# Kernel optimization log

Hardware: AMD Instinct MI355X
Metric: run time of the kernel (lower is better)

The kernel has to match this reference:

```python
import jax, jax.numpy as jnp
import numpy as np

B, C, H, W = 64, 256, 14, 14
K = 9
HID = 256   # EdgeAgg hidden_channels = in_channels
OUT = 512   # out_channels = 2*in_channels (required by final reshape)


def _knn(q, kset, k):
    # ViG dense_knn_matrix: squared-distance knn, top-k of -dist (self-loop may be included)
    qs = jnp.sum(q * q, -1)
    ks = jnp.sum(kset * kset, -1)
    dist = qs[:, :, None] - 2.0 * jnp.einsum('bnc,bmc->bnm', q, kset) + ks[:, None, :]
    _, idx = jax.lax.top_k(-dist, k)   # (B,N,k) neighbor indices into kset
    return idx


def _edgeconv_add(feat, nbr, validf, w, b):
    # PyG EdgeConv(nn=Linear, aggr='add') with per-node valid-edge mask:
    #   out[i] = sum_{j in valid nbrs(i)} cat(x_i, x_j - x_i) @ w + b
    # nn is linear, so aggregate neighbor diffs BEFORE the matmul (same math, less traffic).
    Cf = feat.shape[-1]
    wa, wb = w[:Cf], w[Cf:]
    deg = jnp.sum(validf, -1, keepdims=True)                   # (B,N,1)
    xj = feat[jnp.arange(feat.shape[0])[:, None, None], nbr]   # (B,N,k,C) gather
    sum_xj = jnp.einsum('bnkc,bnk->bnc', xj, validf)
    return deg * (feat @ wa + b) + (sum_xj - deg * feat) @ wb


def _forward(x, fc1_w, fc1_b, fc2_w, fc2_b, fce_w, fce_b, inout_w, inout_b,
             attn_w, attn_b, upd_w, upd_b, kp_w, kp_b, enc_w, enc_b,
             mu_w, mu_b, dec_w, dec_b, T):
    k = dec_w.shape[-1]
    b_, c_, h_, w_ = x.shape
    n = h_ * w_
    xs = x.reshape(b_, c_, n)                       # (B,C,N)
    x_sp = jnp.transpose(xs, (0, 2, 1))             # (B,N,C) true spatial node feats for knn
    x_sp_d = jax.lax.stop_gradient(x_sp)            # original detaches before knn
    x_nbr = _knn(x_sp_d, x_sp_d, k)
    # temporal roll across the T frames of each clip
    y_sp = jnp.roll(x_sp.reshape(b_ // T, T, n, c_), -1, axis=1).reshape(b_, n, c_)
    y_nbr = _knn(x_sp_d, jax.lax.stop_gradient(y_sp), k)
    # faithful to original: x.view(B*N, C) reinterprets the contiguous (B,C,N) buffer
    x_feat = xs.reshape(b_, n, c_)
    y_feat = jnp.transpose(y_sp, (0, 2, 1)).reshape(b_, n, c_)
    # VAE-like K predictor (deterministic z = mu); argmax -> per-node degree in [0,k)
    hk = x_feat.reshape(b_ * n, c_) @ kp_w + kp_b
    hk = jax.nn.relu(hk @ enc_w + enc_b)
    mu = hk @ mu_w + mu_b
    logits = mu @ dec_w + dec_b                     # (B*N, k)
    k_int = jnp.argmax(logits, axis=1)
    # generate_mask: keep the first k_int[i] of node i's k edges
    validf = (jnp.arange(k)[None, :] < k_int[:, None]).astype(x.dtype).reshape(b_, n, k)

    def edge_agg(feat, nbr):
        h1 = jax.nn.relu(_edgeconv_add(feat, nbr, validf, fc1_w, fc1_b))
        h2 = _edgeconv_add(h1, nbr, validf, fc2_w, fc2_b)
        return (h2 @ fce_w + fce_b).reshape(b_ * n, -1)

    x_agg = edge_agg(x_feat, x_nbr)
    y_agg = edge_agg(y_feat, y_nbr)
    scores = (jnp.concatenate([x_agg, y_agg], -1) @ attn_w + attn_b)[:, 0]
    wgt = jax.nn.softmax(scores, axis=0)[:, None]   # softmax over ALL B*N nodes (as in source)
    fused = wgt * x_agg + (1.0 - wgt) * y_agg
    xin = x_feat.reshape(b_ * n, c_) @ inout_w + inout_b
    upd = jax.nn.relu(jnp.concatenate([xin, fused], -1) @ upd_w + upd_b)   # (B*N, 2C)
    return jnp.transpose(upd.reshape(b_, n, 2 * c_), (0, 2, 1)).reshape(b_, 2 * c_, h_, w_)


def setup_inputs():
    key = jax.random.key(0)
    ks = iter(jax.random.split(key, 32))

    def lin(i, o):
        return jax.random.normal(next(ks), (i, o), jnp.float32) / np.sqrt(i)

    def bias(o):
        return jax.random.normal(next(ks), (o,), jnp.float32) * 0.01

    return {
        'x': jax.random.normal(next(ks), (B, C, H, W), jnp.float32),
        'fc1_w': lin(2 * C, HID), 'fc1_b': bias(HID),
        'fc2_w': lin(2 * HID, HID), 'fc2_b': bias(HID),
        'fce_w': lin(HID, OUT), 'fce_b': bias(OUT),
        'inout_w': lin(C, OUT), 'inout_b': bias(OUT),
        'attn_w': lin(2 * OUT, 1), 'attn_b': bias(1),
        'upd_w': lin(2 * OUT, OUT), 'upd_b': bias(OUT),
        'kp_w': lin(C, 500), 'kp_b': bias(500),
        'enc_w': lin(500, 64), 'enc_b': bias(64),
        'mu_w': lin(64, 32), 'mu_b': bias(32),
        'dec_w': lin(32, K), 'dec_b': bias(K),
        'T': 16,
    }


def reference(x, fc1_w, fc1_b, fc2_w, fc2_b, fce_w, fce_b, inout_w, inout_b,
              attn_w, attn_b, upd_w, upd_b, kp_w, kp_b, enc_w, enc_b,
              mu_w, mu_b, dec_w, dec_b, T):
    return _forward(x, fc1_w, fc1_b, fc2_w, fc2_b, fce_w, fce_b, inout_w, inout_b,
                    attn_w, attn_b, upd_w, upd_b, kp_w, kp_b, enc_w, enc_b,
                    mu_w, mu_b, dec_w, dec_b, T)
```

## Files before the change

### kernel.cpp

```cpp
#include <hip/hip_runtime.h>
#include <cstddef>
#include <cstdint>

constexpr int BATCH = 64;
constexpr int CH    = 256;
constexpr int NPT   = 196;
constexpr int ROWS  = BATCH * NPT;
constexpr int BSTRIDE = CH * NPT;
constexpr int KNB   = 8;

typedef __bf16 bf16x8 __attribute__((ext_vector_type(8)));
typedef __bf16 bf16x4 __attribute__((ext_vector_type(4)));
typedef _Float16 f16x8 __attribute__((ext_vector_type(8)));
typedef float  f32x4  __attribute__((ext_vector_type(4)));

__device__ __forceinline__ int src_batch(int b) {
    return (b & ~15) | ((b + 1) & 15);
}

__device__ __forceinline__ void gload_lds16(const void* g, void* l) {
    __builtin_amdgcn_global_load_lds(
        (const __attribute__((address_space(1))) void*)g,
        (__attribute__((address_space(3))) void*)l, 16, 0, 0);
}

__global__ __launch_bounds__(256) void qs_kernel(const float* __restrict__ x,
                                                 float* __restrict__ qs) {
    int b = blockIdx.x;
    int m = threadIdx.x;
    if (m >= NPT) return;
    const float* xb = x + (size_t)b * BSTRIDE;
    float acc = 0.f;
    for (int c = 0; c < CH; ++c) {
        float v = xb[c * NPT + m];
        acc = fmaf(v, v, acc);
    }
    qs[b * NPT + m] = acc;
}

__global__ __launch_bounds__(256) void trans_split(const float* __restrict__ x,
        _Float16* __restrict__ XH, _Float16* __restrict__ XL,
        __bf16* __restrict__ XB) {
    __shared__ float tile[64][65];
    int b = blockIdx.z;
    int m0 = blockIdx.x * 64, c0 = blockIdx.y * 64;
    int t = threadIdx.x;
    const float* xb = x + (size_t)b * BSTRIDE;
    #pragma unroll
    for (int s = 0; s < 16; ++s) {
        int idx = s * 256 + t;
        int cc = idx >> 6, mm = idx & 63;
        int m = m0 + mm;
        float v = (m < NPT) ? xb[(size_t)(c0 + cc) * NPT + m] : 0.f;
        tile[cc][mm] = v;
        if (m < NPT)
            XB[(size_t)b * BSTRIDE + (size_t)(c0 + cc) * NPT + m] = (__bf16)v;
    }
    __syncthreads();
    #pragma unroll
    for (int s = 0; s < 16; ++s) {
        int idx = s * 256 + t;
        int mm = idx >> 6, cc = idx & 63;
        float v = tile[cc][mm];
        _Float16 h = (_Float16)v;
        size_t off = ((size_t)b * 256 + (m0 + mm)) * 256 + c0 + cc;
        XH[off] = h;
        XL[off] = (_Float16)(v - (float)h);
    }
}

__global__ __launch_bounds__(256) void gram_mfma(const _Float16* __restrict__ XH,
        const _Float16* __restrict__ XL, float* __restrict__ D) {
    __shared__ __attribute__((aligned(16))) _Float16 Ah[128 * 64];
    __shared__ __attribute__((aligned(16))) _Float16 Al[128 * 64];
    __shared__ __attribute__((aligned(16))) _Float16 Bh[128 * 64];
    __shared__ __attribute__((aligned(16))) _Float16 Bl[128 * 64];
    int job = blockIdx.z;
    int qb = (job < 64) ? job : job - 64;
    int kb = (job < 64) ? qb : src_batch(qb);
    int t = threadIdx.x, w = t >> 6, l = t & 63;
    int r0 = blockIdx.y * 128, c0 = blockIdx.x * 128;
    int lr = l & 15, lg = l >> 4;
    int wr = (w >> 1) * 64, wc = (w & 1) * 64;
    const _Float16* qh = XH + (size_t)qb * 65536;
    const _Float16* ql = XL + (size_t)qb * 65536;
    const _Float16* kh = XH + (size_t)kb * 65536;
    const _Float16* kl = XL + (size_t)kb * 65536;
    f32x4 acc[4][4] = {};
    for (int k0 = 0; k0 < 256; k0 += 64) {
        #pragma unroll
        for (int i = 0; i < 4; ++i) {
            int row = (w * 4 + i) * 8 + (l >> 3);
            int c8 = l & 7;
            size_t goA = (size_t)(r0 + row) * 256 + k0 + c8 * 8;
            size_t goB = (size_t)(c0 + row) * 256 + k0 + c8 * 8;
            gload_lds16(qh + goA, Ah + (w * 4 + i) * 512);
            gload_lds16(ql + goA, Al + (w * 4 + i) * 512);
            gload_lds16(kh + goB, Bh + (w * 4 + i) * 512);
            gload_lds16(kl + goB, Bl + (w * 4 + i) * 512);
        }
        asm volatile("s_waitcnt vmcnt(0)" ::: "memory");
        __syncthreads();
        #pragma unroll
        for (int ks = 0; ks < 2; ++ks) {
            f16x8 ah[4], al[4], bh[4], bl[4];
            #pragma unroll
            for (int mi = 0; mi < 4; ++mi) {
                ah[mi] = *(const f16x8*)(Ah + (wr + mi * 16 + lr) * 64 + ks * 32 + lg * 8);
                al[mi] = *(const f16x8*)(Al + (wr + mi * 16 + lr) * 64 + ks * 32 + lg * 8);
            }
            #pragma unroll
            for (int ni = 0; ni < 4; ++ni) {
                bh[ni] = *(const f16x8*)(Bh + (wc + ni * 16 + lr) * 64 + ks * 32 + lg * 8);
                bl[ni] = *(const f16x8*)(Bl + (wc + ni * 16 + lr) * 64 + ks * 32 + lg * 8);
            }
            #pragma unroll
            for (int mi = 0; mi < 4; ++mi)
                #pragma unroll
                for (int ni = 0; ni < 4; ++ni) {
                    acc[mi][ni] = __builtin_amdgcn_mfma_f32_16x16x32_f16(
                        ah[mi], bh[ni], acc[mi][ni], 0, 0, 0);
                    acc[mi][ni] = __builtin_amdgcn_mfma_f32_16x16x32_f16(
                        ah[mi], bl[ni], acc[mi][ni], 0, 0, 0);
                    acc[mi][ni] = __builtin_amdgcn_mfma_f32_16x16x32_f16(
                        al[mi], bh[ni], acc[mi][ni], 0, 0, 0);
                }
        }
        __syncthreads();
    }
    #pragma unroll
    for (int mi = 0; mi < 4; ++mi) {
        #pragma unroll
        for (int r = 0; r < 4; ++r) {
            int gi = r0 + wr + mi * 16 + lg * 4 + r;
            if (gi >= NPT) continue;
            #pragma unroll
            for (int ni = 0; ni < 4; ++ni) {
                int gj = c0 + wc + ni * 16 + lr;
                if (gj < NPT)
                    D[(size_t)job * (NPT * NPT) + (size_t)gi * NPT + gj] =
                        acc[mi][ni][r];
            }
        }
    }
}

__global__ __launch_bounds__(256) void topk_kernel(const float* __restrict__ D,
                                                   const float* __restrict__ qs,
                                                   int* __restrict__ nbr) {
    int wid = threadIdx.x >> 6;
    int lane = threadIdx.x & 63;
    int rowid = blockIdx.x * 4 + wid;
    int job = rowid / NPT;
    int i = rowid - job * NPT;
    int qb = (job < 64) ? job : job - 64;
    int kb = (job < 64) ? qb : src_batch(qb);
    const float* drow = D + (size_t)job * (NPT * NPT) + (size_t)i * NPT;
    float qsi = qs[qb * NPT + i];
    const float* ksr = qs + kb * NPT;
    float dist[4];
    #pragma unroll
    for (int s = 0; s < 4; ++s) {
        int m = lane + 64 * s;
        dist[s] = (m < NPT) ? (qsi - 2.f * drow[m] + ksr[m])
                            : __uint_as_float(0x7f800000u);
    }
    for (int it = 0; it < KNB; ++it) {
        unsigned long long best = ~0ull;
        #pragma unroll
        for (int s = 0; s < 4; ++s) {
            unsigned u = __float_as_uint(dist[s]);
            u = (u & 0x80000000u) ? ~u : (u | 0x80000000u);
            unsigned long long key = ((unsigned long long)u << 32) |
                                     (unsigned)(lane + 64 * s);
            if (key < best) best = key;
        }
        #pragma unroll
        for (int off = 32; off; off >>= 1) {
            unsigned long long o = __shfl_xor(best, off, 64);
            if (o < best) best = o;
        }
        int widx = (int)(best & 0xffffffffu);
        if (lane == (widx & 63)) dist[widx >> 6] = __uint_as_float(0x7f800000u);
        if (lane == 0) nbr[(size_t)rowid * KNB + it] = widx;
    }
}

__global__ __launch_bounds__(256) void compose_all(const float* __restrict__ kp_w,
        const float* __restrict__ kp_b, const float* __restrict__ enc_w,
        const float* __restrict__ enc_b, const float* __restrict__ mu_w,
        const float* __restrict__ mu_b, const float* __restrict__ dec_w,
        const float* __restrict__ dec_b, const float* __restrict__ inout_w,
        const float* __restrict__ inout_b, const float* __restrict__ upd_w,
        const float* __restrict__ upd_b,
        float* __restrict__ KW1, float* __restrict__ kb1,
        float* __restrict__ KW2, float* __restrict__ kb2,
        __bf16* __restrict__ updC, float* __restrict__ bcomp) {
    int bid = blockIdx.x;
    if (bid < 64) {
        int i = bid * 4 + (threadIdx.x >> 6);
        int j = threadIdx.x & 63;
        double acc = 0.0;
        for (int k = 0; k < 500; ++k)
            acc += (double)kp_w[(size_t)i * 500 + k] * (double)enc_w[(size_t)k * 64 + j];
        KW1[i * 64 + j] = (float)acc;
    } else if (bid == 64) {
        int j = threadIdx.x;
        if (j < 64) {
            double acc = (double)enc_b[j];
            for (int k = 0; k < 500; ++k)
                acc += (double)kp_b[k] * (double)enc_w[(size_t)k * 64 + j];
            kb1[j] = (float)acc;
        }
    } else if (bid < 68) {
        int t = (bid - 65) * 256 + threadIdx.x;
        if (t < 576) {
            int i = t / 9, j = t - (t / 9) * 9;
            double acc = 0.0;
            for (int k = 0; k < 32; ++k)
                acc += (double)mu_w[(size_t)i * 32 + k] * (double)dec_w[(size_t)k * 9 + j];
            KW2[t] = (float)acc;
        } else if (t < 585) {
            int j = t - 576;
            double acc = (double)dec_b[j];
            for (int k = 0; k < 32; ++k)
                acc += (double)mu_b[k] * (double)dec_w[(size_t)k * 9 + j];
            kb2[j] = (float)acc;
        }
    } else if (bid < 580) {
        int e = (bid - 68) * 256 + threadIdx.x;
        int k = e >> 9, n = e & 511;
        double acc = 0.0;
        for (int j = 0; j < 512; ++j)
            acc += (double)inout_w[(size_t)k * 512 + j] * (double)upd_w[(size_t)j * 512 + n];
        updC[(size_t)n * 768 + k] = (__bf16)(float)acc;
    } else {
        int n = (bid - 580) * 256 + threadIdx.x;
        double acc = (double)upd_b[n];
        for (int j = 0; j < 512; ++j)
            acc += (double)inout_b[j] * (double)upd_w[(size_t)j * 512 + n];
        bcomp[n] = (float)acc;
    }
}

__global__ __launch_bounds__(256) void kint2_kernel(const float* __restrict__ x,
    const float* __restrict__ W1, const float* __restrict__ b1,
    const float* __restrict__ W2, const float* __restrict__ b2,
    int* __restrict__ kint, float* __restrict__ degf) {
    __shared__ __attribute__((aligned(16))) float xr[16][256];
    __shared__ float ebuf[16][64];
    __shared__ float lg[16][9];
    int t = threadIdx.x;
    int r0 = blockIdx.x * 16;
    const float4* xg = (const float4*)(x + (size_t)r0 * 256);
    float4* xs = (float4*)&xr[0][0];
    #pragma unroll
    for (int s = 0; s < 4; ++s) xs[s * 256 + t] = xg[s * 256 + t];
    __syncthreads();
    int w = t >> 6, l = t & 63;
    {
        float bb = b1[l];
        float a0 = bb, a1 = bb, a2 = bb, a3 = bb;
        const float* x0 = xr[w * 4 + 0];
        const float* x1 = xr[w * 4 + 1];
        const float* x2 = xr[w * 4 + 2];
        const float* x3 = xr[w * 4 + 3];
        for (int c = 0; c < 256; ++c) {
            float wv = W1[c * 64 + l];
            a0 = fmaf(x0[c], wv, a0);
            a1 = fmaf(x1[c], wv, a1);
            a2 = fmaf(x2[c], wv, a2);
            a3 = fmaf(x3[c], wv, a3);
        }
        ebuf[w * 4 + 0][l] = fmaxf(a0, 0.f);
        ebuf[w * 4 + 1][l] = fmaxf(a1, 0.f);
        ebuf[w * 4 + 2][l] = fmaxf(a2, 0.f);
        ebuf[w * 4 + 3][l] = fmaxf(a3, 0.f);
    }
    __syncthreads();
    int rr = t >> 4, cc = t & 15;
    if (cc < 9) {
        float acc = b2[cc];
        for (int j = 0; j < 64; ++j)
            acc = fmaf(ebuf[rr][j], W2[j * 9 + cc], acc);
        lg[rr][cc] = acc;
    }
    __syncthreads();
    if (cc == 0) {
        float best = lg[rr][0];
        int bi = 0;
        #pragma unroll
        for (int j = 1; j < 9; ++j)
            if (lg[rr][j] > best) { best = lg[rr][j]; bi = j; }
        kint[r0 + rr] = bi;
        degf[r0 + rr] = (float)bi;
    }
}

template<int STAGE, int RELU>
__global__ __launch_bounds__(256) void combine_kernel(const __bf16* __restrict__ P,
        const int* __restrict__ nbr, const int* __restrict__ kint_,
        const float* __restrict__ degf, const float* __restrict__ bias,
        __bf16* __restrict__ H) {
    int g = threadIdx.x >> 6, lane = threadIdx.x & 63;
    int r = blockIdx.x * 4 + g;
    int branch = (r >= ROWS);
    int rr = r - branch * ROWS;
    int b = rr / NPT, i = rr - b * NPT;
    size_t srow, mbase;
    if constexpr (STAGE == 1) {
        int fb = branch ? src_batch(b) : b;
        srow = (size_t)fb * NPT + i;
        mbase = (size_t)fb * NPT;
    } else {
        srow = (size_t)r;
        mbase = (size_t)branch * ROWS + (size_t)b * NPT;
    }
    const int* nb = nbr + (size_t)branch * ((size_t)ROWS * KNB) + (size_t)rr * KNB;
    bf16x4 sv = *(const bf16x4*)(P + srow * 512 + lane * 4);
    float4 bv = *(const float4*)(bias + lane * 4);
    float s0 = 0.f, s1 = 0.f, s2 = 0.f, s3 = 0.f;
    int kk = kint_[rr];
    for (int tt = 0; tt < kk; ++tt) {
        int m = nb[tt];
        bf16x4 v = *(const bf16x4*)(P + (mbase + m) * 512 + 256 + lane * 4);
        s0 += (float)v[0]; s1 += (float)v[1]; s2 += (float)v[2]; s3 += (float)v[3];
    }
    float dg = degf[rr];
    float o0 = fmaf(dg, (float)sv[0] + bv.x, s0);
    float o1 = fmaf(dg, (float)sv[1] + bv.y, s1);
    float o2 = fmaf(dg, (float)sv[2] + bv.z, s2);
    float o3 = fmaf(dg, (float)sv[3] + bv.w, s3);
    if constexpr (RELU) {
        o0 = fmaxf(o0, 0.f); o1 = fmaxf(o1, 0.f);
        o2 = fmaxf(o2, 0.f); o3 = fmaxf(o3, 0.f);
    }
    bf16x4 ov;
    ov[0] = (__bf16)o0; ov[1] = (__bf16)o1; ov[2] = (__bf16)o2; ov[3] = (__bf16)o3;
    *(bf16x4*)(H + (size_t)r * 256 + lane * 4) = ov;
}

template<int FLAGS, int CONCAT>
__global__ __launch_bounds__(256) void mfma_gemm(
    const __bf16* __restrict__ A0, const __bf16* __restrict__ A1,
    const __bf16* __restrict__ WT, const float* __restrict__ bias,
    float* __restrict__ Cf, __bf16* __restrict__ Cb, int K, int N,
    const float* __restrict__ aw, float* __restrict__ scp,
    const float* __restrict__ wgt) {
    constexpr int SMEMB = (FLAGS & 8) ? (128 * 129 * 4) : (2 * 128 * 64 * 2);
    __shared__ __attribute__((aligned(16))) char smem[SMEMB];
    __bf16* As = (__bf16*)smem;
    __bf16* Bs = As + 128 * 64;
    int t = threadIdx.x, w = t >> 6, l = t & 63;
    int r0 = blockIdx.y * 128, c0 = blockIdx.x * 128;
    int lr = l & 15, lg = l >> 4;
    int wr = (w >> 1) * 64, wc = (w & 1) * 64;
    f32x4 acc[4][4] = {};
    for (int k0 = 0; k0 < K; k0 += 64) {
        #pragma unroll
        for (int i = 0; i < 4; ++i) {
            int row = (w * 4 + i) * 8 + (l >> 3);
            int c8 = l & 7;
            if constexpr (CONCAT == 2) {
                if (k0 < 256) {
                    gload_lds16(A0 + (size_t)(r0 + row) * 256 + k0 + c8 * 8,
                                As + (w * 4 + i) * 512);
                } else {
                    int kk2 = k0 - 256 + c8 * 8;
                    size_t gr = (size_t)(r0 + row);
                    bf16x8 xa = *(const bf16x8*)(A1 + gr * 512 + kk2);
                    bf16x8 ya = *(const bf16x8*)(A1 + ((size_t)ROWS + gr) * 512 + kk2);
                    float wv = wgt[gr];
                    bf16x8 mx;
                    #pragma unroll
                    for (int j = 0; j < 8; ++j)
                        mx[j] = (__bf16)(wv * (float)xa[j] + (1.f - wv) * (float)ya[j]);
                    *(bf16x8*)(As + (w * 4 + i) * 512 + l * 8) = mx;
                }
            } else {
                gload_lds16(A0 + (size_t)(r0 + row) * K + k0 + c8 * 8,
                            As + (w * 4 + i) * 512);
            }
            gload_lds16(WT + (size_t)(c0 + row) * K + k0 + c8 * 8,
                        Bs + (w * 4 + i) * 512);
        }
        asm volatile("s_waitcnt vmcnt(0)" ::: "memory");
        __syncthreads();
        #pragma unroll
        for (int ks = 0; ks < 2; ++ks) {
            bf16x8 af[4], bfr[4];
            #pragma unroll
            for (int mi = 0; mi < 4; ++mi)
                af[mi] = *(const bf16x8*)(As + (wr + mi * 16 + lr) * 64 + ks * 32 + lg * 8);
            #pragma unroll
            for (int ni = 0; ni < 4; ++ni)
                bfr[ni] = *(const bf16x8*)(Bs + (wc + ni * 16 + lr) * 64 + ks * 32 + lg * 8);
            #pragma unroll
            for (int mi = 0; mi < 4; ++mi)
                #pragma unroll
                for (int ni = 0; ni < 4; ++ni)
                    acc[mi][ni] = __builtin_amdgcn_mfma_f32_16x16x32_bf16(
                        af[mi], bfr[ni], acc[mi][ni], 0, 0, 0);
        }
        __syncthreads();
    }
    if constexpr ((FLAGS & 8) != 0) {
        float* tile = (float*)smem;
        #pragma unroll
        for (int mi = 0; mi < 4; ++mi)
            #pragma unroll
            for (int r = 0; r < 4; ++r) {
                int rrow = wr + mi * 16 + lg * 4 + r;
                #pragma unroll
                for (int ni = 0; ni < 4; ++ni) {
                    int ccol = wc + ni * 16 + lr;
                    float v = acc[mi][ni][r];
                    if (bias) v += bias[c0 + ccol];
                    if constexpr ((FLAGS & 1) != 0) v = fmaxf(v, 0.f);
                    tile[rrow * 129 + ccol] = v;
                }
            }
        __syncthreads();
        int cc = t >> 6, rr2 = t & 63;
        #pragma unroll
        for (int cs = 0; cs < 128; cs += 4) {
            #pragma unroll
            for (int h = 0; h < 2; ++h) {
                int row = r0 + rr2 + h * 64;
                int bb = row / NPT, ii = row - bb * NPT;
                Cf[((size_t)bb * 512 + (c0 + cc + cs)) * NPT + ii] =
                    tile[(rr2 + h * 64) * 129 + cc + cs];
            }
        }
    } else if constexpr ((FLAGS & 16) != 0) {
        int half = (r0 >= ROWS) ? 1 : 0;
        float ps[4][4] = {};
        #pragma unroll
        for (int mi = 0; mi < 4; ++mi)
            #pragma unroll
            for (int r = 0; r < 4; ++r) {
                int row = r0 + wr + mi * 16 + lg * 4 + r;
                #pragma unroll
                for (int ni = 0; ni < 4; ++ni) {
                    int col = c0 + wc + ni * 16 + lr;
                    float v = acc[mi][ni][r] + bias[col];
                    Cb[(size_t)row * N + col] = (__bf16)v;
                    ps[mi][r] = fmaf(v, aw[half * 512 + col], ps[mi][r]);
                }
            }
        #pragma unroll
        for (int m = 1; m <= 8; m <<= 1)
            #pragma unroll
            for (int mi = 0; mi < 4; ++mi)
                #pragma unroll
                for (int r = 0; r < 4; ++r)
                    ps[mi][r] += __shfl_xor(ps[mi][r], m, 64);
        if (lr == 0) {
            int slot = half * 8 + blockIdx.x * 2 + (w & 1);
            #pragma unroll
            for (int mi = 0; mi < 4; ++mi)
                #pragma unroll
                for (int r = 0; r < 4; ++r) {
                    int sr = r0 - half * ROWS + wr + mi * 16 + lg * 4 + r;
                    scp[(size_t)slot * ROWS + sr] = ps[mi][r];
                }
        }
    } else {
        #pragma unroll
        for (int mi = 0; mi < 4; ++mi) {
            #pragma unroll
            for (int r = 0; r < 4; ++r) {
                int row = r0 + wr + mi * 16 + lg * 4 + r;
                #pragma unroll
                for (int ni = 0; ni < 4; ++ni) {
                    int col = c0 + wc + ni * 16 + lr;
                    float v = acc[mi][ni][r];
                    if (bias) v += bias[col];
                    if constexpr ((FLAGS & 1) != 0) v = fmaxf(v, 0.f);
                    if constexpr ((FLAGS & 4) != 0)
                        Cb[(size_t)row * N + col] = (__bf16)v;
                    else
                        Cf[(size_t)row * N + col] = v;
                }
            }
        }
    }
}

__global__ __launch_bounds__(256) void transpose_all(
        const float* __restrict__ fc1_w, const float* __restrict__ fc2_w,
        const float* __restrict__ fce_w, const float* __restrict__ upd_w,
        __bf16* __restrict__ W1catT, __bf16* __restrict__ W2catT,
        __bf16* __restrict__ fcet, __bf16* __restrict__ updC) {
    __shared__ float tile[64][65];
    int bid = blockIdx.x;
    int t = threadIdx.x;
    if (bid < 64) {
        const float* W = (bid < 32) ? fc1_w : fc2_w;
        __bf16* WT = (bid < 32) ? W1catT : W2catT;
        int local = bid & 31;
        int n0 = (local >> 2) * 64, k0 = (local & 3) * 64;
        #pragma unroll
        for (int s = 0; s < 16; ++s) {
            int idx = s * 256 + t;
            int kk = idx >> 6, nn = idx & 63;
            float v;
            if (n0 < 256)
                v = W[(size_t)(k0 + kk) * 256 + n0 + nn] -
                    W[(size_t)(k0 + kk + 256) * 256 + n0 + nn];
            else
                v = W[(size_t)(k0 + kk + 256) * 256 + (n0 - 256) + nn];
            tile[kk][nn] = v;
        }
        __syncthreads();
        #pragma unroll
        for (int s = 0; s < 16; ++s) {
            int idx = s * 256 + t;
            int nn = idx >> 6, kk = idx & 63;
            WT[(size_t)(n0 + nn) * 256 + k0 + kk] = (__bf16)tile[kk][nn];
        }
    } else if (bid < 96) {
        int local = bid - 64;
        int n0 = (local >> 2) * 64, k0 = (local & 3) * 64;
        #pragma unroll
        for (int s = 0; s < 16; ++s) {
            int idx = s * 256 + t;
            int kk = idx >> 6, nn = idx & 63;
            tile[kk][nn] = fce_w[(size_t)(k0 + kk) * 512 + n0 + nn];
        }
        __syncthreads();
        #pragma unroll
        for (int s = 0; s < 16; ++s) {
            int idx = s * 256 + t;
            int nn = idx >> 6, kk = idx & 63;
            fcet[(size_t)(n0 + nn) * 256 + k0 + kk] = (__bf16)tile[kk][nn];
        }
    } else {
        int local = bid - 96;
        int k0 = (local >> 3) * 64, n0 = (local & 7) * 64;
        #pragma unroll
        for (int s = 0; s < 16; ++s) {
            int idx = s * 256 + t;
            int kk = idx >> 6, nn = idx & 63;
            tile[kk][nn] = upd_w[(size_t)(512 + k0 + kk) * 512 + n0 + nn];
        }
        __syncthreads();
        #pragma unroll
        for (int s = 0; s < 16; ++s) {
            int idx = s * 256 + t;
            int nn = idx >> 6, kk = idx & 63;
            updC[(size_t)(n0 + nn) * 768 + 256 + k0 + kk] = (__bf16)tile[kk][nn];
        }
    }
}

__global__ __launch_bounds__(256) void softmax_part(const float* __restrict__ scp,
        const float* __restrict__ ab, float* __restrict__ scores,
        float* __restrict__ mpart, float* __restrict__ spart) {
    __shared__ float red[256];
    int t = threadIdx.x;
    int sr = blockIdx.x * 256 + t;
    float s = ab[0];
    #pragma unroll
    for (int i = 0; i < 16; ++i) s += scp[(size_t)i * ROWS + sr];
    scores[sr] = s;
    red[t] = s; __syncthreads();
    for (int off = 128; off; off >>= 1) {
        if (t < off) red[t] = fmaxf(red[t], red[t + off]);
        __syncthreads();
    }
    float mb = red[0]; __syncthreads();
    red[t] = expf(s - mb); __syncthreads();
    for (int off = 128; off; off >>= 1) {
        if (t < off) red[t] += red[t + off];
        __syncthreads();
    }
    if (t == 0) { mpart[blockIdx.x] = mb; spart[blockIdx.x] = red[0]; }
}

__global__ __launch_bounds__(256) void softmax_fin(const float* __restrict__ mpart,
        const float* __restrict__ spart, const float* __restrict__ scores,
        float* __restrict__ wgt) {
    __shared__ float MS[2];
    if (threadIdx.x == 0) {
        float M = mpart[0];
        for (int i = 1; i < 49; ++i) M = fmaxf(M, mpart[i]);
        float S = 0.f;
        for (int i = 0; i < 49; ++i) S += spart[i] * expf(mpart[i] - M);
        MS[0] = M; MS[1] = S;
    }
    __syncthreads();
    float M = MS[0], denom = MS[1];
    for (int i = threadIdx.x; i < ROWS; i += 256)
        wgt[i] = expf(scores[i] - M) / denom;
}

extern "C" void kernel_launch(void* const* d_in, const int* in_sizes, int n_in,
                              void* d_out, int out_size, void* d_ws, size_t ws_size,
                              hipStream_t stream) {
    (void)in_sizes; (void)n_in; (void)out_size; (void)ws_size;
    const float* x       = (const float*)d_in[0];
    const float* fc1_w   = (const float*)d_in[1];
    const float* fc1_b   = (const float*)d_in[2];
    const float* fc2_w   = (const float*)d_in[3];
    const float* fc2_b   = (const float*)d_in[4];
    const float* fce_w   = (const float*)d_in[5];
    const float* fce_b   = (const float*)d_in[6];
    const float* inout_w = (const float*)d_in[7];
    const float* inout_b = (const float*)d_in[8];
    const float* attn_w  = (const float*)d_in[9];
    const float* attn_b  = (const float*)d_in[10];
    const float* upd_w   = (const float*)d_in[11];
    const float* upd_b   = (const float*)d_in[12];
    const float* kp_w    = (const float*)d_in[13];
    const float* kp_b    = (const float*)d_in[14];
    const float* enc_w   = (const float*)d_in[15];
    const float* enc_b   = (const float*)d_in[16];
    const float* mu_w    = (const float*)d_in[17];
    const float* mu_b    = (const float*)d_in[18];
    const float* dec_w   = (const float*)d_in[19];
    const float* dec_b   = (const float*)d_in[20];
    float* out = (float*)d_out;

    char* base = (char*)d_ws;
    size_t o = 0;
    auto alloc = [&](size_t bytes) -> void* {
        void* p = base + o;
        o += (bytes + 255) & ~(size_t)255;
        return p;
    };
    float* qs     = (float*)alloc(ROWS * 4);
    float* degf   = (float*)alloc(ROWS * 4);
    float* scores = (float*)alloc(ROWS * 4);
    float* wgt    = (float*)alloc(ROWS * 4);
    int*   kint   = (int*)  alloc(ROWS * 4);
    float* KW1    = (float*)alloc(256 * 64 * 4);
    float* kb1    = (float*)alloc(64 * 4);
    float* KW2    = (float*)alloc(64 * 9 * 4);
    float* kb2    = (float*)alloc(9 * 4);
    float* bcomp  = (float*)alloc(512 * 4);
    float* scp    = (float*)alloc((size_t)16 * ROWS * 4);
    float* mpart  = (float*)alloc(64 * 4);
    float* spart  = (float*)alloc(64 * 4);
    int*   nbr    = (int*)  alloc((size_t)128 * NPT * KNB * 4);
    char*  regD   = (char*) alloc((size_t)128 * NPT * NPT * 4);
    __bf16* XB    = (__bf16*)alloc((size_t)ROWS * 256 * 2);
    __bf16* H1    = (__bf16*)alloc((size_t)2 * ROWS * 256 * 2);
    __bf16* H2    = (__bf16*)alloc((size_t)2 * ROWS * 256 * 2);
    char*  regAGG = (char*) alloc((size_t)2 * ROWS * 512 * 4);
    __bf16* W1catT= (__bf16*)alloc((size_t)512 * 256 * 2);
    __bf16* W2catT= (__bf16*)alloc((size_t)512 * 256 * 2);
    __bf16* fcet  = (__bf16*)alloc((size_t)512 * 256 * 2);
    __bf16* updC  = (__bf16*)alloc((size_t)512 * 768 * 2);
    float*  D     = (float*)regD;
    __bf16* P1buf = (__bf16*)regD;
    _Float16* XSPH = (_Float16*)regAGG;
    _Float16* XSPL = XSPH + (size_t)64 * 256 * 256;
    __bf16* P2buf = (__bf16*)regAGG;
    __bf16* AGGb  = (__bf16*)regAGG;
    __bf16* XAGGb = AGGb;

    transpose_all<<<160, 256, 0, stream>>>(fc1_w, fc2_w, fce_w, upd_w,
                                           W1catT, W2catT, fcet, updC);
    compose_all<<<582, 256, 0, stream>>>(kp_w, kp_b, enc_w, enc_b,
                                         mu_w, mu_b, dec_w, dec_b,
                                         inout_w, inout_b, upd_w, upd_b,
                                         KW1, kb1, KW2, kb2, updC, bcomp);
    qs_kernel<<<64, 256, 0, stream>>>(x, qs);
    trans_split<<<dim3(4, 4, 64), 256, 0, stream>>>(x, XSPH, XSPL, XB);

    gram_mfma<<<dim3(2, 2, 128), 256, 0, stream>>>(XSPH, XSPL, D);
    topk_kernel<<<(128 * NPT) / 4, 256, 0, stream>>>(D, qs, nbr);
    kint2_kernel<<<ROWS / 16, 256, 0, stream>>>(x, KW1, kb1, KW2, kb2, kint, degf);

    mfma_gemm<4, 0><<<dim3(4, 98), 256, 0, stream>>>(
        XB, nullptr, W1catT, nullptr, nullptr, P1buf, 256, 512,
        nullptr, nullptr, nullptr);
    combine_kernel<1, 1><<<2 * ROWS / 4, 256, 0, stream>>>(
        P1buf, nbr, kint, degf, fc1_b, H1);

    mfma_gemm<4, 0><<<dim3(4, 196), 256, 0, stream>>>(
        H1, nullptr, W2catT, nullptr, nullptr, P2buf, 256, 512,
        nullptr, nullptr, nullptr);
    combine_kernel<2, 0><<<2 * ROWS / 4, 256, 0, stream>>>(
        P2buf, nbr, kint, degf, fc2_b, H2);

    mfma_gemm<20, 0><<<dim3(4, 196), 256, 0, stream>>>(
        H2, nullptr, fcet, fce_b, nullptr, AGGb, 256, 512,
        attn_w, scp, nullptr);

    softmax_part<<<49, 256, 0, stream>>>(scp, attn_b, scores, mpart, spart);
    softmax_fin<<<1, 256, 0, stream>>>(mpart, spart, scores, wgt);

    mfma_gemm<9, 2><<<dim3(4, 98), 256, 0, stream>>>(
        XB, XAGGb, updC, bcomp, out, nullptr, 768, 512,
        nullptr, nullptr, wgt);
}
```

Measured before the change: 259.3 us.

## Fuse kNN top-k into gram epilogue, merge prep kernels, add XCD swizzle

Computes distances and per-64-column partial top-8 candidates inside the gram MFMA epilogue, so the full distance matrix is no longer written and re-read. A small merge kernel then combines four sorted candidate lists per row. Separate weight-prep, qs, transpose-split and K-predictor kernels are folded into two multi-role launches to cut launch count. XCD-aware block swizzling is added to the gram, GEMM and combine kernels for cache locality. The epilogue now carries extra shuffle and register work, and the merge relies on the per-tile candidate lists being sorted.

```diff
diff --git a/kernel.cpp b/kernel.cpp
--- a/kernel.cpp
+++ b/kernel.cpp
@@ -13,6 +13,7 @@
 typedef __bf16 bf16x4 __attribute__((ext_vector_type(4)));
 typedef _Float16 f16x8 __attribute__((ext_vector_type(8)));
 typedef float  f32x4  __attribute__((ext_vector_type(4)));
+typedef unsigned long long u64;
 
 __device__ __forceinline__ int src_batch(int b) {
     return (b & ~15) | ((b + 1) & 15);
@@ -24,62 +25,122 @@
         (__attribute__((address_space(3))) void*)l, 16, 0, 0);
 }
 
-__global__ __launch_bounds__(256) void qs_kernel(const float* __restrict__ x,
-                                                 float* __restrict__ qs) {
-    int b = blockIdx.x;
-    int m = threadIdx.x;
-    if (m >= NPT) return;
-    const float* xb = x + (size_t)b * BSTRIDE;
-    float acc = 0.f;
-    for (int c = 0; c < CH; ++c) {
-        float v = xb[c * NPT + m];
-        acc = fmaf(v, v, acc);
-    }
-    qs[b * NPT + m] = acc;
-}
-
-__global__ __launch_bounds__(256) void trans_split(const float* __restrict__ x,
+__device__ __forceinline__ int xcd_swz(int lin, int nwg) {
+    int q = nwg >> 3;
+    return (lin & 7) * q + (lin >> 3);
+}
+
+__global__ __launch_bounds__(256) void front_kernel(const float* __restrict__ x,
         _Float16* __restrict__ XH, _Float16* __restrict__ XL,
-        __bf16* __restrict__ XB) {
-    __shared__ float tile[64][65];
-    int b = blockIdx.z;
-    int m0 = blockIdx.x * 64, c0 = blockIdx.y * 64;
+        __bf16* __restrict__ XB, float* __restrict__ qs,
+        const float* __restrict__ W1, const float* __restrict__ b1,
+        const float* __restrict__ W2, const float* __restrict__ b2,
+        int* __restrict__ kint, float* __restrict__ degf) {
+    __shared__ __attribute__((aligned(16))) char smem[21056];
+    int bid = blockIdx.x;
     int t = threadIdx.x;
-    const float* xb = x + (size_t)b * BSTRIDE;
-    #pragma unroll
-    for (int s = 0; s < 16; ++s) {
-        int idx = s * 256 + t;
-        int cc = idx >> 6, mm = idx & 63;
-        int m = m0 + mm;
-        float v = (m < NPT) ? xb[(size_t)(c0 + cc) * NPT + m] : 0.f;
-        tile[cc][mm] = v;
-        if (m < NPT)
-            XB[(size_t)b * BSTRIDE + (size_t)(c0 + cc) * NPT + m] = (__bf16)v;
-    }
-    __syncthreads();
-    #pragma unroll
-    for (int s = 0; s < 16; ++s) {
-        int idx = s * 256 + t;
-        int mm = idx >> 6, cc = idx & 63;
-        float v = tile[cc][mm];
-        _Float16 h = (_Float16)v;
-        size_t off = ((size_t)b * 256 + (m0 + mm)) * 256 + c0 + cc;
-        XH[off] = h;
-        XL[off] = (_Float16)(v - (float)h);
+    if (bid < 1024) {
+        float (*tile)[65] = (float(*)[65])smem;
+        int m0 = (bid & 3) * 64, c0 = ((bid >> 2) & 3) * 64, b = bid >> 4;
+        const float* xb = x + (size_t)b * BSTRIDE;
+        #pragma unroll
+        for (int s = 0; s < 16; ++s) {
+            int idx = s * 256 + t;
+            int cc = idx >> 6, mm = idx & 63;
+            int m = m0 + mm;
+            float v = (m < NPT) ? xb[(size_t)(c0 + cc) * NPT + m] : 0.f;
+            tile[cc][mm] = v;
+            if (m < NPT)
+                XB[(size_t)b * BSTRIDE + (size_t)(c0 + cc) * NPT + m] = (__bf16)v;
+        }
+        __syncthreads();
+        #pragma unroll
+        for (int s = 0; s < 16; ++s) {
+            int idx = s * 256 + t;
+            int mm = idx >> 6, cc = idx & 63;
+            float v = tile[cc][mm];
+            _Float16 h = (_Float16)v;
+            size_t off = ((size_t)b * 256 + (m0 + mm)) * 256 + c0 + cc;
+            XH[off] = h;
+            XL[off] = (_Float16)(v - (float)h);
+        }
+    } else if (bid < 1088) {
+        int b = bid - 1024;
+        int m = t;
+        if (m >= NPT) return;
+        const float* xb = x + (size_t)b * BSTRIDE;
+        float acc = 0.f;
+        for (int c = 0; c < CH; ++c) {
+            float v = xb[c * NPT + m];
+            acc = fmaf(v, v, acc);
+        }
+        qs[b * NPT + m] = acc;
+    } else {
+        float (*xr)[256] = (float(*)[256])smem;
+        float (*ebuf)[64] = (float(*)[64])(smem + 16384);
+        float (*lg)[9]   = (float(*)[9])(smem + 20480);
+        int r0 = (bid - 1088) * 16;
+        const float4* xg = (const float4*)(x + (size_t)r0 * 256);
+        float4* xs = (float4*)&xr[0][0];
+        #pragma unroll
+        for (int s = 0; s < 4; ++s) xs[s * 256 + t] = xg[s * 256 + t];
+        __syncthreads();
+        int w = t >> 6, l = t & 63;
+        {
+            float bb = b1[l];
+            float a0 = bb, a1 = bb, a2 = bb, a3 = bb;
+            const float* x0 = xr[w * 4 + 0];
+            const float* x1 = xr[w * 4 + 1];
+            const float* x2 = xr[w * 4 + 2];
+            const float* x3 = xr[w * 4 + 3];
+            for (int c = 0; c < 256; ++c) {
+                float wv = W1[c * 64 + l];
+                a0 = fmaf(x0[c], wv, a0);
+                a1 = fmaf(x1[c], wv, a1);
+                a2 = fmaf(x2[c], wv, a2);
+                a3 = fmaf(x3[c], wv, a3);
+            }
+            ebuf[w * 4 + 0][l] = fmaxf(a0, 0.f);
+            ebuf[w * 4 + 1][l] = fmaxf(a1, 0.f);
+            ebuf[w * 4 + 2][l] = fmaxf(a2, 0.f);
+            ebuf[w * 4 + 3][l] = fmaxf(a3, 0.f);
+        }
+        __syncthreads();
+        int rr = t >> 4, cc = t & 15;
+        if (cc < 9) {
+            float acc = b2[cc];
+            for (int j = 0; j < 64; ++j)
+                acc = fmaf(ebuf[rr][j], W2[j * 9 + cc], acc);
+            lg[rr][cc] = acc;
+        }
+        __syncthreads();
+        if (cc == 0) {
+            float best = lg[rr][0];
+            int bi = 0;
+            #pragma unroll
+            for (int j = 1; j < 9; ++j)
+                if (lg[rr][j] > best) { best = lg[rr][j]; bi = j; }
+            kint[r0 + rr] = bi;
+            degf[r0 + rr] = (float)bi;
+        }
     }
 }
 
 __global__ __launch_bounds__(256) void gram_mfma(const _Float16* __restrict__ XH,
-        const _Float16* __restrict__ XL, float* __restrict__ D) {
+        const _Float16* __restrict__ XL, const float* __restrict__ qs,
+        u64* __restrict__ cand) {
     __shared__ __attribute__((aligned(16))) _Float16 Ah[128 * 64];
     __shared__ __attribute__((aligned(16))) _Float16 Al[128 * 64];
     __shared__ __attribute__((aligned(16))) _Float16 Bh[128 * 64];
     __shared__ __attribute__((aligned(16))) _Float16 Bl[128 * 64];
-    int job = blockIdx.z;
+    int lin = blockIdx.x + 2 * blockIdx.y + 4 * blockIdx.z;
+    int nid = xcd_swz(lin, 512);
+    int bx = nid & 1, by = (nid >> 1) & 1;
+    int job = nid >> 2;
     int qb = (job < 64) ? job : job - 64;
     int kb = (job < 64) ? qb : src_batch(qb);
     int t = threadIdx.x, w = t >> 6, l = t & 63;
-    int r0 = blockIdx.y * 128, c0 = blockIdx.x * 128;
+    int r0 = by * 128, c0 = bx * 128;
     int lr = l & 15, lg = l >> 4;
     int wr = (w >> 1) * 64, wc = (w & 1) * 64;
     const _Float16* qh = XH + (size_t)qb * 65536;
@@ -128,172 +189,193 @@
         }
         __syncthreads();
     }
+    const float* qsq = qs + qb * NPT;
+    const float* qsk = qs + kb * NPT;
+    int tile = (c0 + wc) >> 6;
+    float ksv[4];
+    #pragma unroll
+    for (int ni = 0; ni < 4; ++ni) {
+        int col = c0 + wc + ni * 16 + lr;
+        ksv[ni] = (col < NPT) ? qsk[col] : 0.f;
+    }
     #pragma unroll
     for (int mi = 0; mi < 4; ++mi) {
         #pragma unroll
         for (int r = 0; r < 4; ++r) {
-            int gi = r0 + wr + mi * 16 + lg * 4 + r;
-            if (gi >= NPT) continue;
+            int row = r0 + wr + mi * 16 + lg * 4 + r;
+            bool rowvalid = row < NPT;
+            float qq = rowvalid ? qsq[row] : 0.f;
+            u64 key[4];
             #pragma unroll
             for (int ni = 0; ni < 4; ++ni) {
-                int gj = c0 + wc + ni * 16 + lr;
-                if (gj < NPT)
-                    D[(size_t)job * (NPT * NPT) + (size_t)gi * NPT + gj] =
-                        acc[mi][ni][r];
-            }
-        }
-    }
-}
-
-__global__ __launch_bounds__(256) void topk_kernel(const float* __restrict__ D,
-                                                   const float* __restrict__ qs,
-                                                   int* __restrict__ nbr) {
-    int wid = threadIdx.x >> 6;
-    int lane = threadIdx.x & 63;
-    int rowid = blockIdx.x * 4 + wid;
-    int job = rowid / NPT;
-    int i = rowid - job * NPT;
-    int qb = (job < 64) ? job : job - 64;
-    int kb = (job < 64) ? qb : src_batch(qb);
-    const float* drow = D + (size_t)job * (NPT * NPT) + (size_t)i * NPT;
-    float qsi = qs[qb * NPT + i];
-    const float* ksr = qs + kb * NPT;
-    float dist[4];
+                int col = c0 + wc + ni * 16 + lr;
+                float dist = qq - 2.f * acc[mi][ni][r] + ksv[ni];
+                unsigned u = __float_as_uint(dist);
+                u = (u & 0x80000000u) ? ~u : (u | 0x80000000u);
+                key[ni] = (col < NPT) ? (((u64)u << 32) | (unsigned)col) : ~0ull;
+            }
+            u64 outk[8];
+            #pragma unroll
+            for (int it = 0; it < 8; ++it) {
+                u64 best = key[0];
+                #pragma unroll
+                for (int ni = 1; ni < 4; ++ni)
+                    best = (key[ni] < best) ? key[ni] : best;
+                #pragma unroll
+                for (int m = 1; m <= 8; m <<= 1) {
+                    u64 o = __shfl_xor(best, m, 64);
+                    if (o < best) best = o;
+                }
+                outk[it] = best;
+                #pragma unroll
+                for (int ni = 0; ni < 4; ++ni)
+                    if (key[ni] == best) key[ni] = ~0ull;
+            }
+            if (rowvalid && lr == 0) {
+                u64* cp = cand + (((size_t)job * NPT + row) * 4 + tile) * 8;
+                #pragma unroll
+                for (int it = 0; it < 8; ++it) cp[it] = outk[it];
+            }
+        }
+    }
+}
+
+__global__ __launch_bounds__(256) void topk_merge(const u64* __restrict__ cand,
+                                                  int* __restrict__ nbr) {
+    int rowid = blockIdx.x * 256 + threadIdx.x;
+    const u64* c = cand + (size_t)rowid * 32;
+    int p0 = 0, p1 = 0, p2 = 0, p3 = 0;
     #pragma unroll
-    for (int s = 0; s < 4; ++s) {
-        int m = lane + 64 * s;
-        dist[s] = (m < NPT) ? (qsi - 2.f * drow[m] + ksr[m])
-                            : __uint_as_float(0x7f800000u);
-    }
-    for (int it = 0; it < KNB; ++it) {
-        unsigned long long best = ~0ull;
-        #pragma unroll
-        for (int s = 0; s < 4; ++s) {
-            unsigned u = __float_as_uint(dist[s]);
-            u = (u & 0x80000000u) ? ~u : (u | 0x80000000u);
-            unsigned long long key = ((unsigned long long)u << 32) |
-                                     (unsigned)(lane + 64 * s);
-            if (key < best) best = key;
-        }
-        #pragma unroll
-        for (int off = 32; off; off >>= 1) {
-            unsigned long long o = __shfl_xor(best, off, 64);
-            if (o < best) best = o;
-        }
-        int widx = (int)(best & 0xffffffffu);
-        if (lane == (widx & 63)) dist[widx >> 6] = __uint_as_float(0x7f800000u);
-        if (lane == 0) nbr[(size_t)rowid * KNB + it] = widx;
-    }
-}
-
-__global__ __launch_bounds__(256) void compose_all(const float* __restrict__ kp_w,
-        const float* __restrict__ kp_b, const float* __restrict__ enc_w,
-        const float* __restrict__ enc_b, const float* __restrict__ mu_w,
-        const float* __restrict__ mu_b, const float* __restrict__ dec_w,
-        const float* __restrict__ dec_b, const float* __restrict__ inout_w,
-        const float* __restrict__ inout_b, const float* __restrict__ upd_w,
+    for (int it = 0; it < 8; ++it) {
+        u64 v0 = c[p0], v1 = c[8 + p1], v2 = c[16 + p2], v3 = c[24 + p3];
+        u64 best = v0; int bj = 0;
+        if (v1 < best) { best = v1; bj = 1; }
+        if (v2 < best) { best = v2; bj = 2; }
+        if (v3 < best) { best = v3; bj = 3; }
+        if (bj == 0) p0 = (p0 < 7) ? p0 + 1 : 7;
+        else if (bj == 1) p1 = (p1 < 7) ? p1 + 1 : 7;
+        else if (bj == 2) p2 = (p2 < 7) ? p2 + 1 : 7;
+        else p3 = (p3 < 7) ? p3 + 1 : 7;
+        nbr[(size_t)rowid * KNB + it] = (int)(best & 0xffffffffu);
+    }
+}
+
+__global__ __launch_bounds__(256) void prep_weights(
+        const float* __restrict__ fc1_w, const float* __restrict__ fc2_w,
+        const float* __restrict__ fce_w, const float* __restrict__ upd_w,
+        const float* __restrict__ kp_w, const float* __restrict__ kp_b,
+        const float* __restrict__ enc_w, const float* __restrict__ enc_b,
+        const float* __restrict__ mu_w, const float* __restrict__ mu_b,
+        const float* __restrict__ dec_w, const float* __restrict__ dec_b,
+        const float* __restrict__ inout_w, const float* __restrict__ inout_b,
         const float* __restrict__ upd_b,
+        __bf16* __restrict__ W1catT, __bf16* __restrict__ W2catT,
+        __bf16* __restrict__ fcet, __bf16* __restrict__ updC,
         float* __restrict__ KW1, float* __restrict__ kb1,
         float* __restrict__ KW2, float* __restrict__ kb2,
-        __bf16* __restrict__ updC, float* __restrict__ bcomp) {
+        float* __restrict__ bcomp) {
+    __shared__ float tile[64][65];
     int bid = blockIdx.x;
+    int t = threadIdx.x;
     if (bid < 64) {
-        int i = bid * 4 + (threadIdx.x >> 6);
-        int j = threadIdx.x & 63;
+        const float* W = (bid < 32) ? fc1_w : fc2_w;
+        __bf16* WT = (bid < 32) ? W1catT : W2catT;
+        int local = bid & 31;
+        int n0 = (local >> 2) * 64, k0 = (local & 3) * 64;
+        #pragma unroll
+        for (int s = 0; s < 16; ++s) {
+            int idx = s * 256 + t;
+            int kk = idx >> 6, nn = idx & 63;
+            float v;
+            if (n0 < 256)
+                v = W[(size_t)(k0 + kk) * 256 + n0 + nn] -
+                    W[(size_t)(k0 + kk + 256) * 256 + n0 + nn];
+            else
+                v = W[(size_t)(k0 + kk + 256) * 256 + (n0 - 256) + nn];
+            tile[kk][nn] = v;
+        }
+        __syncthreads();
+        #pragma unroll
+        for (int s = 0; s < 16; ++s) {
+            int idx = s * 256 + t;
+            int nn = idx >> 6, kk = idx & 63;
+            WT[(size_t)(n0 + nn) * 256 + k0 + kk] = (__bf16)tile[kk][nn];
+        }
+    } else if (bid < 96) {
+        int local = bid - 64;
+        int n0 = (local >> 2) * 64, k0 = (local & 3) * 64;
+        #pragma unroll
+        for (int s = 0; s < 16; ++s) {
+            int idx = s * 256 + t;
+            int kk = idx >> 6, nn = idx & 63;
+            tile[kk][nn] = fce_w[(size_t)(k0 + kk) * 512 + n0 + nn];
+        }
+        __syncthreads();
+        #pragma unroll
+        for (int s = 0; s < 16; ++s) {
+            int idx = s * 256 + t;
+            int nn = idx >> 6, kk = idx & 63;
+            fcet[(size_t)(n0 + nn) * 256 + k0 + kk] = (__bf16)tile[kk][nn];
+        }
+    } else if (bid < 160) {
+        int local = bid - 96;
+        int k0 = (local >> 3) * 64, n0 = (local & 7) * 64;
+        #pragma unroll
+        for (int s = 0; s < 16; ++s) {
+            int idx = s * 256 + t;
+            int kk = idx >> 6, nn = idx & 63;
+            tile[kk][nn] = upd_w[(size_t)(512 + k0 + kk) * 512 + n0 + nn];
+        }
+        __syncthreads();
+        #pragma unroll
+        for (int s = 0; s < 16; ++s) {
+            int idx = s * 256 + t;
+            int nn = idx >> 6, kk = idx & 63;
+            updC[(size_t)(n0 + nn) * 768 + 256 + k0 + kk] = (__bf16)tile[kk][nn];
+        }
+    } else if (bid < 224) {
+        int i = (bid - 160) * 4 + (t >> 6);
+        int j = t & 63;
         double acc = 0.0;
         for (int k = 0; k < 500; ++k)
             acc += (double)kp_w[(size_t)i * 500 + k] * (double)enc_w[(size_t)k * 64 + j];
         KW1[i * 64 + j] = (float)acc;
-    } else if (bid == 64) {
-        int j = threadIdx.x;
+    } else if (bid == 224) {
+        int j = t;
         if (j < 64) {
             double acc = (double)enc_b[j];
             for (int k = 0; k < 500; ++k)
                 acc += (double)kp_b[k] * (double)enc_w[(size_t)k * 64 + j];
             kb1[j] = (float)acc;
         }
-    } else if (bid < 68) {
-        int t = (bid - 65) * 256 + threadIdx.x;
-        if (t < 576) {
-            int i = t / 9, j = t - (t / 9) * 9;
+    } else if (bid < 228) {
+        int e = (bid - 225) * 256 + t;
+        if (e < 576) {
+            int i = e / 9, j = e - (e / 9) * 9;
             double acc = 0.0;
             for (int k = 0; k < 32; ++k)
                 acc += (double)mu_w[(size_t)i * 32 + k] * (double)dec_w[(size_t)k * 9 + j];
-            KW2[t] = (float)acc;
-        } else if (t < 585) {
-            int j = t - 576;
+            KW2[e] = (float)acc;
+        } else if (e < 585) {
+            int j = e - 576;
             double acc = (double)dec_b[j];
             for (int k = 0; k < 32; ++k)
                 acc += (double)mu_b[k] * (double)dec_w[(size_t)k * 9 + j];
             kb2[j] = (float)acc;
         }
-    } else if (bid < 580) {
-        int e = (bid - 68) * 256 + threadIdx.x;
+    } else if (bid < 740) {
+        int e = (bid - 228) * 256 + t;
         int k = e >> 9, n = e & 511;
         double acc = 0.0;
         for (int j = 0; j < 512; ++j)
             acc += (double)inout_w[(size_t)k * 512 + j] * (double)upd_w[(size_t)j * 512 + n];
         updC[(size_t)n * 768 + k] = (__bf16)(float)acc;
     } else {
-        int n = (bid - 580) * 256 + threadIdx.x;
+        int n = (bid - 740) * 256 + t;
         double acc = (double)upd_b[n];
         for (int j = 0; j < 512; ++j)
             acc += (double)inout_b[j] * (double)upd_w[(size_t)j * 512 + n];
         bcomp[n] = (float)acc;
-    }
-}
-
-__global__ __launch_bounds__(256) void kint2_kernel(const float* __restrict__ x,
-    const float* __restrict__ W1, const float* __restrict__ b1,
-    const float* __restrict__ W2, const float* __restrict__ b2,
-    int* __restrict__ kint, float* __restrict__ degf) {
-    __shared__ __attribute__((aligned(16))) float xr[16][256];
-    __shared__ float ebuf[16][64];
-    __shared__ float lg[16][9];
-    int t = threadIdx.x;
-    int r0 = blockIdx.x * 16;
-    const float4* xg = (const float4*)(x + (size_t)r0 * 256);
-    float4* xs = (float4*)&xr[0][0];
-    #pragma unroll
-    for (int s = 0; s < 4; ++s) xs[s * 256 + t] = xg[s * 256 + t];
-    __syncthreads();
-    int w = t >> 6, l = t & 63;
-    {
-        float bb = b1[l];
-        float a0 = bb, a1 = bb, a2 = bb, a3 = bb;
-        const float* x0 = xr[w * 4 + 0];
-        const float* x1 = xr[w * 4 + 1];
-        const float* x2 = xr[w * 4 + 2];
-        const float* x3 = xr[w * 4 + 3];
-        for (int c = 0; c < 256; ++c) {
-            float wv = W1[c * 64 + l];
-            a0 = fmaf(x0[c], wv, a0);
-            a1 = fmaf(x1[c], wv, a1);
-            a2 = fmaf(x2[c], wv, a2);
-            a3 = fmaf(x3[c], wv, a3);
-        }
-        ebuf[w * 4 + 0][l] = fmaxf(a0, 0.f);
-        ebuf[w * 4 + 1][l] = fmaxf(a1, 0.f);
-        ebuf[w * 4 + 2][l] = fmaxf(a2, 0.f);
-        ebuf[w * 4 + 3][l] = fmaxf(a3, 0.f);
-    }
-    __syncthreads();
-    int rr = t >> 4, cc = t & 15;
-    if (cc < 9) {
-        float acc = b2[cc];
-        for (int j = 0; j < 64; ++j)
-            acc = fmaf(ebuf[rr][j], W2[j * 9 + cc], acc);
-        lg[rr][cc] = acc;
-    }
-    __syncthreads();
-    if (cc == 0) {
-        float best = lg[rr][0];
-        int bi = 0;
-        #pragma unroll
-        for (int j = 1; j < 9; ++j)
-            if (lg[rr][j] > best) { best = lg[rr][j]; bi = j; }
-        kint[r0 + rr] = bi;
-        degf[r0 + rr] = (float)bi;
     }
 }
 
@@ -303,7 +385,8 @@
         const float* __restrict__ degf, const float* __restrict__ bias,
         __bf16* __restrict__ H) {
     int g = threadIdx.x >> 6, lane = threadIdx.x & 63;
-    int r = blockIdx.x * 4 + g;
+    int nid = xcd_swz(blockIdx.x, 2 * ROWS / 4);
+    int r = nid * 4 + g;
     int branch = (r >= ROWS);
     int rr = r - branch * ROWS;
     int b = rr / NPT, i = rr - b * NPT;
@@ -351,8 +434,11 @@
     __shared__ __attribute__((aligned(16))) char smem[SMEMB];
     __bf16* As = (__bf16*)smem;
     __bf16* Bs = As + 128 * 64;
+    int lin = blockIdx.x + 4 * blockIdx.y;
+    int nid = xcd_swz(lin, 4 * gridDim.y);
+    int bx = nid & 3, by = nid >> 2;
     int t = threadIdx.x, w = t >> 6, l = t & 63;
-    int r0 = blockIdx.y * 128, c0 = blockIdx.x * 128;
+    int r0 = by * 128, c0 = bx * 128;
     int lr = l & 15, lg = l >> 4;
     int wr = (w >> 1) * 64, wc = (w & 1) * 64;
     f32x4 acc[4][4] = {};
@@ -456,7 +542,7 @@
                 for (int r = 0; r < 4; ++r)
                     ps[mi][r] += __shfl_xor(ps[mi][r], m, 64);
         if (lr == 0) {
-            int slot = half * 8 + blockIdx.x * 2 + (w & 1);
+            int slot = half * 8 + bx * 2 + (w & 1);
             #pragma unroll
             for (int mi = 0; mi < 4; ++mi)
                 #pragma unroll
@@ -483,73 +569,6 @@
                         Cf[(size_t)row * N + col] = v;
                 }
             }
-        }
-    }
-}
-
-__global__ __launch_bounds__(256) void transpose_all(
-        const float* __restrict__ fc1_w, const float* __restrict__ fc2_w,
-        const float* __restrict__ fce_w, const float* __restrict__ upd_w,
-        __bf16* __restrict__ W1catT, __bf16* __restrict__ W2catT,
-        __bf16* __restrict__ fcet, __bf16* __restrict__ updC) {
-    __shared__ float tile[64][65];
-    int bid = blockIdx.x;
-    int t = threadIdx.x;
-    if (bid < 64) {
-        const float* W = (bid < 32) ? fc1_w : fc2_w;
-        __bf16* WT = (bid < 32) ? W1catT : W2catT;
-        int local = bid & 31;
-        int n0 = (local >> 2) * 64, k0 = (local & 3) * 64;
-        #pragma unroll
-        for (int s = 0; s < 16; ++s) {
-            int idx = s * 256 + t;
-            int kk = idx >> 6, nn = idx & 63;
-            float v;
-            if (n0 < 256)
-                v = W[(size_t)(k0 + kk) * 256 + n0 + nn] -
-                    W[(size_t)(k0 + kk + 256) * 256 + n0 + nn];
-            else
-                v = W[(size_t)(k0 + kk + 256) * 256 + (n0 - 256) + nn];
-            tile[kk][nn] = v;
-        }
-        __syncthreads();
-        #pragma unroll
-        for (int s = 0; s < 16; ++s) {
-            int idx = s * 256 + t;
-            int nn = idx >> 6, kk = idx & 63;
-            WT[(size_t)(n0 + nn) * 256 + k0 + kk] = (__bf16)tile[kk][nn];
-        }
-    } else if (bid < 96) {
-        int local = bid - 64;
-        int n0 = (local >> 2) * 64, k0 = (local & 3) * 64;
-        #pragma unroll
-        for (int s = 0; s < 16; ++s) {
-            int idx = s * 256 + t;
-            int kk = idx >> 6, nn = idx & 63;
-            tile[kk][nn] = fce_w[(size_t)(k0 + kk) * 512 + n0 + nn];
-        }
-        __syncthreads();
-        #pragma unroll
-        for (int s = 0; s < 16; ++s) {
-            int idx = s * 256 + t;
-            int nn = idx >> 6, kk = idx & 63;
-            fcet[(size_t)(n0 + nn) * 256 + k0 + kk] = (__bf16)tile[kk][nn];
-        }
-    } else {
-        int local = bid - 96;
-        int k0 = (local >> 3) * 64, n0 = (local & 7) * 64;
-        #pragma unroll
-        for (int s = 0; s < 16; ++s) {
-            int idx = s * 256 + t;
-            int kk = idx >> 6, nn = idx & 63;
-            tile[kk][nn] = upd_w[(size_t)(512 + k0 + kk) * 512 + n0 + nn];
-        }
-        __syncthreads();
-        #pragma unroll
-        for (int s = 0; s < 16; ++s) {
-            int idx = s * 256 + t;
-            int nn = idx >> 6, kk = idx & 63;
-            updC[(size_t)(n0 + nn) * 768 + 256 + k0 + kk] = (__bf16)tile[kk][nn];
         }
     }
 }
@@ -643,7 +662,8 @@
     float* mpart  = (float*)alloc(64 * 4);
     float* spart  = (float*)alloc(64 * 4);
     int*   nbr    = (int*)  alloc((size_t)128 * NPT * KNB * 4);
-    char*  regD   = (char*) alloc((size_t)128 * NPT * NPT * 4);
+    u64*   cand   = (u64*)  alloc((size_t)128 * NPT * 4 * 8 * 8);
+    char*  regD   = (char*) alloc((size_t)ROWS * 512 * 2);
     __bf16* XB    = (__bf16*)alloc((size_t)ROWS * 256 * 2);
     __bf16* H1    = (__bf16*)alloc((size_t)2 * ROWS * 256 * 2);
     __bf16* H2    = (__bf16*)alloc((size_t)2 * ROWS * 256 * 2);
@@ -652,7 +672,6 @@
     __bf16* W2catT= (__bf16*)alloc((size_t)512 * 256 * 2);
     __bf16* fcet  = (__bf16*)alloc((size_t)512 * 256 * 2);
     __bf16* updC  = (__bf16*)alloc((size_t)512 * 768 * 2);
-    float*  D     = (float*)regD;
     __bf16* P1buf = (__bf16*)regD;
     _Float16* XSPH = (_Float16*)regAGG;
     _Float16* XSPL = XSPH + (size_t)64 * 256 * 256;
@@ -660,18 +679,17 @@
     __bf16* AGGb  = (__bf16*)regAGG;
     __bf16* XAGGb = AGGb;
 
-    transpose_all<<<160, 256, 0, stream>>>(fc1_w, fc2_w, fce_w, upd_w,
-                                           W1catT, W2catT, fcet, updC);
-    compose_all<<<582, 256, 0, stream>>>(kp_w, kp_b, enc_w, enc_b,
-                                         mu_w, mu_b, dec_w, dec_b,
-                                         inout_w, inout_b, upd_w, upd_b,
-                                         KW1, kb1, KW2, kb2, updC, bcomp);
-    qs_kernel<<<64, 256, 0, stream>>>(x, qs);
-    trans_split<<<dim3(4, 4, 64), 256, 0, stream>>>(x, XSPH, XSPL, XB);
-
-    gram_mfma<<<dim3(2, 2, 128), 256, 0, stream>>>(XSPH, XSPL, D);
-    topk_kernel<<<(128 * NPT) / 4, 256, 0, stream>>>(D, qs, nbr);
-    kint2_kernel<<<ROWS / 16, 256, 0, stream>>>(x, KW1, kb1, KW2, kb2, kint, degf);
+    prep_weights<<<742, 256, 0, stream>>>(fc1_w, fc2_w, fce_w, upd_w,
+                                          kp_w, kp_b, enc_w, enc_b,
+                                          mu_w, mu_b, dec_w, dec_b,
+                                          inout_w, inout_b, upd_b,
+                                          W1catT, W2catT, fcet, updC,
+                                          KW1, kb1, KW2, kb2, bcomp);
+    front_kernel<<<1872, 256, 0, stream>>>(x, XSPH, XSPL, XB, qs,
+                                           KW1, kb1, KW2, kb2, kint, degf);
+
+    gram_mfma<<<dim3(2, 2, 128), 256, 0, stream>>>(XSPH, XSPL, qs, cand);
+    topk_merge<<<98, 256, 0, stream>>>(cand, nbr);
 
     mfma_gemm<4, 0><<<dim3(4, 98), 256, 0, stream>>>(
         XB, nullptr, W1catT, nullptr, nullptr, P1buf, 256, 512,
```

Result: faster. 242.8 us (-6.4%).
